# Kernel tuning notes

Measured on AMD Instinct MI355X. Metric: run time of the kernel, lower is better.

## Reference

```python
import jax, jax.numpy as jnp
import numpy as np

PAD, BOS, EOS = 0, 1, 2
VOCAB, EMB, HID, BATCH, MAXLEN = 32, 64, 1024, 2048, 100


def setup_inputs() -> dict:
    key = jax.random.key(0)
    ks = jax.random.split(key, 11)
    s = 0.08  # small init scale keeps softmax/sigmoid in a sane range
    g = lambda k, shape: (s * jax.random.normal(k, shape)).astype(jnp.float32)
    emb = g(ks[0], (VOCAB, EMB)).at[PAD].set(0.0)  # padding_idx row = 0
    return {
        "prevs": jnp.full((BATCH, 1), BOS, dtype=jnp.int32),
        "emb": emb,
        "Wih0": g(ks[1], (4 * HID, EMB)),
        "Whh0": g(ks[2], (4 * HID, HID)),
        "bih0": g(ks[3], (4 * HID,)),
        "bhh0": g(ks[4], (4 * HID,)),
        "Wih1": g(ks[5], (4 * HID, HID)),
        "Whh1": g(ks[6], (4 * HID, HID)),
        "bih1": g(ks[7], (4 * HID,)),
        "bhh1": g(ks[8], (4 * HID,)),
        "Wout": g(ks[9], (VOCAB, HID)),
        "bout": g(ks[10], (VOCAB,)),
        "max_len": MAXLEN,
    }


def _lstm_cell(x, h, c, Wih, Whh, bih, bhh):
    # torch LSTM gate order: i, f, g, o
    gates = x @ Wih.T + bih + h @ Whh.T + bhh  # [n, 4H]
    i, f, g, o = jnp.split(gates, 4, axis=-1)
    c = jax.nn.sigmoid(f) * c + jax.nn.sigmoid(i) * jnp.tanh(g)
    h = jax.nn.sigmoid(o) * jnp.tanh(c)
    return h, c


def reference(prevs, emb, Wih0, Whh0, bih0, bhh0, Wih1, Whh1, bih1, bhh1,
              Wout, bout, max_len):
    n = prevs.shape[0]
    H = Whh0.shape[1]
    prev = prevs[:, 0].astype(jnp.int32)
    h0 = jnp.zeros((n, H), jnp.float32)
    c0 = jnp.zeros((n, H), jnp.float32)
    h1 = jnp.zeros((n, H), jnp.float32)
    c1 = jnp.zeros((n, H), jnp.float32)
    is_end = prev == EOS
    lengths = jnp.zeros((n,), jnp.int32)
    keys = jax.random.split(jax.random.key(42), max_len)

    def step(carry, k):
        prev, h0, c0, h1, c1, is_end, lengths = carry
        x = emb[prev]                                   # [n, E]
        h0, c0 = _lstm_cell(x, h0, c0, Wih0, Whh0, bih0, bhh0)
        h1, c1 = _lstm_cell(h0, h1, c1, Wih1, Whh1, bih1, bhh1)
        logits = h1 @ Wout.T + bout                     # [n, V]
        cur = jax.random.categorical(k, logits).astype(jnp.int32)
        cur = jnp.where(is_end, PAD, cur)               # finished rows emit PAD
        lengths = lengths + (~is_end).astype(jnp.int32)
        is_end = is_end | (cur == EOS)
        return (cur, h0, c0, h1, c1, is_end, lengths), cur

    carry, seq = jax.lax.scan(step, (prev, h0, c0, h1, c1, is_end, lengths), keys)
    lengths = carry[6] + 1                               # +1 for BOS, as in sample_tensor
    sequences = jnp.concatenate([prevs.astype(jnp.int32), seq.T], axis=1)  # [n, 1+max_len]
    return sequences, lengths
```

## Files before the change

### kernel.cpp

```cpp
#include <hip/hip_runtime.h>
#include <cstdint>
#include <cstddef>


constexpr int PAD_TOK = 0, BOS_TOK = 1, EOS_TOK = 2;
constexpr int VOCAB = 32, EMB = 64, HID = 1024, BATCH = 2048, MAXLEN = 100;
constexpr int BK = 32;
constexpr int NKT_H = HID / BK;
constexpr float SCALE = 64.0f;
constexpr double INV_S2 = 1.0 / 4096.0;

using half8 = __attribute__((ext_vector_type(8))) _Float16;
using f32x4 = __attribute__((ext_vector_type(4))) float;
typedef unsigned short u16;
typedef uint32_t u32;

__device__ __forceinline__ u32 rotl32(u32 v, int d) {
  return (v << d) | (v >> (32 - d));
}

__device__ __forceinline__ void threefry2x32(u32 k0, u32 k1, u32 x0, u32 x1,
                                             u32& y0, u32& y1) {
  const u32 k2 = k0 ^ k1 ^ 0x1BD11BDAu;
#define TF_ROUND(r) do { x0 += x1; x1 = rotl32(x1, (r)); x1 ^= x0; } while (0)
  x0 += k0; x1 += k1;
  TF_ROUND(13); TF_ROUND(15); TF_ROUND(26); TF_ROUND(6);
  x0 += k1; x1 += k2 + 1u;
  TF_ROUND(17); TF_ROUND(29); TF_ROUND(16); TF_ROUND(24);
  x0 += k2; x1 += k0 + 2u;
  TF_ROUND(13); TF_ROUND(15); TF_ROUND(26); TF_ROUND(6);
  x0 += k0; x1 += k1 + 3u;
  TF_ROUND(17); TF_ROUND(29); TF_ROUND(16); TF_ROUND(24);
  x0 += k1; x1 += k2 + 4u;
  TF_ROUND(13); TF_ROUND(15); TF_ROUND(26); TF_ROUND(6);
  x0 += k2; x1 += k0 + 5u;
#undef TF_ROUND
  y0 = x0; y1 = x1;
}

__device__ __forceinline__ double rcp1p(double q) {
  const double d = 1.0 + q;
  double r = (double)__builtin_amdgcn_rcpf((float)d);
  r = r * fma(-d, r, 2.0);
  r = r * fma(-d, r, 2.0);
  return r;
}
__device__ __forceinline__ double exp2d(double t) {
  const double n = rint(t);
  const double f = t - n;
  double p = 1.0178086009239699e-07;
  p = fma(p, f, 1.3215542443841225e-06);
  p = fma(p, f, 1.5252733804059840e-05);
  p = fma(p, f, 1.5403530393381610e-04);
  p = fma(p, f, 1.3333558146428443e-03);
  p = fma(p, f, 9.6181291076284772e-03);
  p = fma(p, f, 5.5504108664821580e-02);
  p = fma(p, f, 2.4022650695910071e-01);
  p = fma(p, f, 6.9314718055994531e-01);
  p = fma(p, f, 1.0);
  const long long e = ((long long)(int)n + 1023) << 52;
  return p * __longlong_as_double(e);
}
__device__ __forceinline__ double sigd(double x) {
  return rcp1p(exp2d(x * -1.4426950408889634));
}
__device__ __forceinline__ double tanhd(double x) {
  return fma(2.0, rcp1p(exp2d(x * -2.8853900817779268)), -1.0);
}

__global__ __launch_bounds__(256) void pack_w(
    const float* __restrict__ src, int K, int nkt,
    uint4* __restrict__ dhi, uint4* __restrict__ dlo, int nchunks) {
  const int g = blockIdx.x * 256 + threadIdx.x;
  if (g >= nchunks) return;
  const int ut = g / (nkt * 512);
  const int rem = g - ut * (nkt * 512);
  const int kt = rem >> 9;
  const int slot = rem & 511;
  const int fm = slot >> 6, kg = (slot >> 4) & 3, r15 = slot & 15;
  const int row = (fm & 3) * HID + ut * 32 + (fm >> 2) * 16 + r15;
  const int col = kt * 32 + kg * 8;
  const float* s = src + (size_t)row * K + col;
  u16 hh[8], ll[8];
#pragma unroll
  for (int e = 0; e < 8; ++e) {
    const float x = s[e] * SCALE;
    const _Float16 h = (_Float16)x;
    const float rm = x - (float)h;
    const _Float16 l = (_Float16)rm;
    hh[e] = __builtin_bit_cast(u16, h);
    ll[e] = __builtin_bit_cast(u16, l);
  }
  dhi[g] = make_uint4((u32)hh[0] | ((u32)hh[1] << 16),
                      (u32)hh[2] | ((u32)hh[3] << 16),
                      (u32)hh[4] | ((u32)hh[5] << 16),
                      (u32)hh[6] | ((u32)hh[7] << 16));
  dlo[g] = make_uint4((u32)ll[0] | ((u32)ll[1] << 16),
                      (u32)ll[2] | ((u32)ll[3] << 16),
                      (u32)ll[4] | ((u32)ll[5] << 16),
                      (u32)ll[6] | ((u32)ll[7] << 16));
}

__global__ __launch_bounds__(256) void split_kernel(
    const float* __restrict__ src, u16* __restrict__ hi, u16* __restrict__ lo,
    int n) {
  const int i = blockIdx.x * 256 + threadIdx.x;
  if (i >= n) return;
  const float x = src[i] * SCALE;
  const _Float16 h = (_Float16)x;
  const float rem = x - (float)h;
  const _Float16 l = (_Float16)rem;
  hi[i] = __builtin_bit_cast(u16, h);
  lo[i] = __builtin_bit_cast(u16, l);
}

__global__ __launch_bounds__(256) void init_kernel(
    const int* __restrict__ prevs, float* __restrict__ c0,
    float* __restrict__ c1, u16* __restrict__ h0hi0, u16* __restrict__ h0lo0,
    u16* __restrict__ h0hi1, u16* __restrict__ h0lo1,
    u16* __restrict__ h1hi0, u16* __restrict__ h1lo0,
    u16* __restrict__ h1hi1, u16* __restrict__ h1lo1,
    int* __restrict__ prev, int* __restrict__ is_end,
    int* __restrict__ lengths, u32* __restrict__ keys,
    int* __restrict__ out_tok) {
  const int tid = blockIdx.x * 256 + threadIdx.x;
  const int total = BATCH * HID;
  if (tid < total) {
    c0[tid] = 0.0f; c1[tid] = 0.0f;
    h0hi0[tid] = 0; h0lo0[tid] = 0; h0hi1[tid] = 0; h0lo1[tid] = 0;
    h1hi0[tid] = 0; h1lo0[tid] = 0; h1hi1[tid] = 0; h1lo1[tid] = 0;
  }
  if (tid < BATCH) {
    const int p = prevs[tid];
    prev[tid] = p;
    is_end[tid] = (p == EOS_TOK) ? 1 : 0;
    lengths[tid] = 0;
    out_tok[(size_t)tid * (MAXLEN + 1)] = p;
  }
  if (tid < MAXLEN) {
    u32 y0, y1;
    threefry2x32(0u, 42u, 0u, (u32)tid, y0, y1);
    keys[2 * tid] = y0;
    keys[2 * tid + 1] = y1;
  }
}

template <bool GATHER, bool WRITE_F32>
__global__ __launch_bounds__(512, 2) void lstm_mfma(
    const uint4* __restrict__ A0p_hi, const uint4* __restrict__ A0p_lo,
    const u16* __restrict__ Ehi, const u16* __restrict__ Elo,
    const int* __restrict__ ptok, int nk0,
    const uint4* __restrict__ A1p_hi, const uint4* __restrict__ A1p_lo,
    const uint4* __restrict__ W0hi, const uint4* __restrict__ W0lo,
    const uint4* __restrict__ W1hi, const uint4* __restrict__ W1lo,
    const float* __restrict__ bih, const float* __restrict__ bhh,
    float* __restrict__ Cst, float* __restrict__ Hf32,
    uint4* __restrict__ Hp_hi, uint4* __restrict__ Hp_lo) {
  __shared__ uint4 lds4[2560];
  char* lds = (char*)lds4;

  const int tid = threadIdx.x;
  const int lane = tid & 63;
  const int wid = tid >> 6;
  const int wm = wid >> 1, wn = wid & 1;

  const int bid = blockIdx.x;
  const int mt = bid & 7;
  const int ut = bid >> 3;
  const int u0 = ut * 32;
  const int row0 = mt * 256;

  const int r15 = lane & 15;
  const int kgrp = lane >> 4;

  int tok4[4];
  if (GATHER) {
#pragma unroll
    for (int mi = 0; mi < 4; ++mi)
      tok4[mi] = ptok[row0 + (wm * 4 + mi) * 16 + r15];
  }

  const int NT = nk0 + NKT_H;

  auto loadT = [&](int kt, uint4* Ah, uint4* Al, uint4* Bh, uint4* Bl) {
    const bool s0 = kt < nk0;
    const int ktl = s0 ? kt : kt - nk0;
    const uint4* wh = s0 ? W0hi : W1hi;
    const uint4* wl = s0 ? W0lo : W1lo;
    const int wb = (ut * (s0 ? nk0 : NKT_H) + ktl) * 512 + wn * 256 + lane;
#pragma unroll
    for (int ni = 0; ni < 4; ++ni) {
      Bh[ni] = wh[wb + ni * 64];
      Bl[ni] = wl[wb + ni * 64];
    }
    if (GATHER && s0) {
#pragma unroll
      for (int mi = 0; mi < 4; ++mi) {
        const size_t ao = (size_t)tok4[mi] * EMB + ktl * 32 + kgrp * 8;
        Ah[mi] = *(const uint4*)(Ehi + ao);
        Al[mi] = *(const uint4*)(Elo + ao);
      }
    } else {
      const uint4* ah_ = s0 ? A0p_hi : A1p_hi;
      const uint4* al_ = s0 ? A0p_lo : A1p_lo;
      const int ab = (mt * NKT_H + ktl) * 1024 + wm * 256 + lane;
#pragma unroll
      for (int mi = 0; mi < 4; ++mi) {
        Ah[mi] = ah_[ab + mi * 64];
        Al[mi] = al_[ab + mi * 64];
      }
    }
  };

  f32x4 acc[4][4] = {};

  auto computeT = [&](const uint4* AhF, const uint4* AlF, const uint4* BhF,
                      const uint4* BlF) {
    half8 ah[4], al[4], bh[4], bl[4];
#pragma unroll
    for (int i = 0; i < 4; ++i) {
      ah[i] = __builtin_bit_cast(half8, AhF[i]);
      al[i] = __builtin_bit_cast(half8, AlF[i]);
      bh[i] = __builtin_bit_cast(half8, BhF[i]);
      bl[i] = __builtin_bit_cast(half8, BlF[i]);
    }
#pragma unroll
    for (int ni = 0; ni < 4; ++ni)
#pragma unroll
      for (int mi = 0; mi < 4; ++mi)
        acc[mi][ni] = __builtin_amdgcn_mfma_f32_16x16x32_f16(
            ah[mi], bh[ni], acc[mi][ni], 0, 0, 0);
#pragma unroll
    for (int ni = 0; ni < 4; ++ni)
#pragma unroll
      for (int mi = 0; mi < 4; ++mi)
        acc[mi][ni] = __builtin_amdgcn_mfma_f32_16x16x32_f16(
            ah[mi], bl[ni], acc[mi][ni], 0, 0, 0);
#pragma unroll
    for (int ni = 0; ni < 4; ++ni)
#pragma unroll
      for (int mi = 0; mi < 4; ++mi)
        acc[mi][ni] = __builtin_amdgcn_mfma_f32_16x16x32_f16(
            al[mi], bh[ni], acc[mi][ni], 0, 0, 0);
  };

  uint4 Ah0[4], Al0[4], Bh0[4], Bl0[4];
  uint4 Ah1[4], Al1[4], Bh1[4], Bl1[4];
  loadT(0, Ah0, Al0, Bh0, Bl0);
  loadT(1, Ah1, Al1, Bh1, Bl1);
#pragma unroll 1
  for (int t = 0; t < NT; t += 2) {
    computeT(Ah0, Al0, Bh0, Bl0);
    if (t + 2 < NT) loadT(t + 2, Ah0, Al0, Bh0, Bl0);
    computeT(Ah1, Al1, Bh1, Bl1);
    if (t + 3 < NT) loadT(t + 3, Ah1, Al1, Bh1, Bl1);
  }

  const int u_loc = wn * 16 + r15;
  const int u = u0 + u_loc;
  double bsum[4];
#pragma unroll
  for (int g = 0; g < 4; ++g)
    bsum[g] = (double)bih[g * HID + u] + (double)bhh[g * HID + u];

  float* Cb = Cst + (size_t)(mt * 32 + ut) * 8192;
  u16* hhT = (u16*)lds;
  u16* hlT = (u16*)(lds + 20480);
  const int hi4 = lane >> 4;

#pragma unroll
  for (int mi = 0; mi < 4; ++mi) {
#pragma unroll
    for (int r = 0; r < 4; ++r) {
      const int row = wm * 64 + mi * 16 + hi4 * 4 + r;
      const double gI = (double)acc[mi][0][r] * INV_S2 + bsum[0];
      const double gF = (double)acc[mi][1][r] * INV_S2 + bsum[1];
      const double gG = (double)acc[mi][2][r] * INV_S2 + bsum[2];
      const double gO = (double)acc[mi][3][r] * INV_S2 + bsum[3];
      const double ii = sigd(gI);
      const double ff = sigd(gF);
      const double gt = tanhd(gG);
      const double oo = sigd(gO);
      const int co = row * 32 + u_loc;
      const double cn = ff * (double)Cb[co] + ii * gt;
      Cb[co] = (float)cn;
      const float hf = (float)(oo * tanhd(cn));
      if (WRITE_F32) Hf32[(size_t)(row0 + row) * HID + u] = hf;
      const float hs = hf * SCALE;
      const _Float16 hh = (_Float16)hs;
      const float rm = hs - (float)hh;
      const _Float16 hl = (_Float16)rm;
      hhT[row * 40 + u_loc] = __builtin_bit_cast(u16, hh);
      hlT[row * 40 + u_loc] = __builtin_bit_cast(u16, hl);
    }
  }
  __syncthreads();

  const size_t mtut = ((size_t)mt * NKT_H + ut) * 1024;
#pragma unroll
  for (int j = 0; j < 2; ++j) {
    const int g = tid + j * 512;
    const int fA = g >> 6, kg = (g >> 4) & 3, rr = g & 15;
    const int row = fA * 16 + rr;
    const uint4 vh = *(const uint4*)(hhT + row * 40 + kg * 8);
    const uint4 vl = *(const uint4*)(hlT + row * 40 + kg * 8);
    Hp_hi[mtut + g] = vh;
    Hp_lo[mtut + g] = vl;
  }
}

__global__ __launch_bounds__(256) void sample_kernel(
    const float* __restrict__ h1, const float* __restrict__ Wout,
    const float* __restrict__ bout, const u32* __restrict__ keys, int t,
    int* __restrict__ prev, int* __restrict__ is_end, int* __restrict__ lengths,
    int* __restrict__ out_tok, int* __restrict__ len_out) {
  const int wave = threadIdx.x >> 6;
  const int lane = threadIdx.x & 63;
  const int row = (blockIdx.x & 7) * 256 + (blockIdx.x >> 3) * 4 + wave;
  const int v = lane & 31;
  const int half = lane >> 5;

  const float* hseg = h1 + (size_t)row * HID + half * (HID / 2);
  const float* wseg = Wout + (size_t)v * HID + half * (HID / 2);

  double acc = 0.0;
#pragma unroll 4
  for (int k = 0; k < HID / 2; k += 4) {
    const float4 w = *(const float4*)(wseg + k);
    const float4 h = *(const float4*)(hseg + k);
    acc = fma((double)w.x, (double)h.x, acc);
    acc = fma((double)w.y, (double)h.y, acc);
    acc = fma((double)w.z, (double)h.z, acc);
    acc = fma((double)w.w, (double)h.w, acc);
  }
  acc += __shfl_xor(acc, 32);

  const u32 k0 = keys[2 * t], k1 = keys[2 * t + 1];
  u32 y0, y1;
  threefry2x32(k0, k1, 0u, (u32)(row * VOCAB + v), y0, y1);
  const u32 bits = y0 ^ y1;
  const float f = __uint_as_float((bits >> 9) | 0x3f800000u) - 1.0f;
  const float uu = fmaxf(f, 1.17549435e-38f);
  const double g = -log(-log((double)uu));

  double z = acc + (double)bout[v] + g;
  int idx = v;
#pragma unroll
  for (int m = 1; m < 32; m <<= 1) {
    const double zo = __shfl_xor(z, m);
    const int io = __shfl_xor(idx, m);
    if (zo > z || (zo == z && io < idx)) { z = zo; idx = io; }
  }

  if (lane == 0) {
    const int e = is_end[row];
    const int cur = e ? PAD_TOK : idx;
    const int len = lengths[row] + (e ? 0 : 1);
    const int enew = e | (cur == EOS_TOK ? 1 : 0);
    prev[row] = cur;
    is_end[row] = enew;
    lengths[row] = len;
    out_tok[(size_t)row * (MAXLEN + 1) + t + 1] = cur;
    if (len_out) len_out[row] = len + 1;
  }
}

extern "C" void kernel_launch(void* const* d_in, const int* in_sizes, int n_in,
                              void* d_out, int out_size, void* d_ws,
                              size_t ws_size, hipStream_t stream) {
  const int* prevs = (const int*)d_in[0];
  const float* emb = (const float*)d_in[1];
  const float* Wih0 = (const float*)d_in[2];
  const float* Whh0 = (const float*)d_in[3];
  const float* bih0 = (const float*)d_in[4];
  const float* bhh0 = (const float*)d_in[5];
  const float* Wih1 = (const float*)d_in[6];
  const float* Whh1 = (const float*)d_in[7];
  const float* bih1 = (const float*)d_in[8];
  const float* bhh1 = (const float*)d_in[9];
  const float* Wout = (const float*)d_in[10];
  const float* bout = (const float*)d_in[11];

  const size_t SH = (size_t)BATCH * HID;
  const size_t CH = SH / 8;
  const size_t CW = (size_t)32 * NKT_H * 512;
  const size_t CW0 = (size_t)32 * 2 * 512;

  float* c0 = (float*)d_ws;
  float* c1 = c0 + SH;
  float* h1f = c1 + SH;
  uint4* q = (uint4*)(h1f + SH);
  uint4* ph0hi[2] = {q, q + CH};
  uint4* ph0lo[2] = {q + 2 * CH, q + 3 * CH};
  uint4* ph1hi[2] = {q + 4 * CH, q + 5 * CH};
  uint4* ph1lo[2] = {q + 6 * CH, q + 7 * CH};
  uint4* pw = q + 8 * CH;
  uint4* pwih0h = pw;              uint4* pwih0l = pwih0h + CW0;
  uint4* pwhh0h = pwih0l + CW0;    uint4* pwhh0l = pwhh0h + CW;
  uint4* pwih1h = pwhh0l + CW;     uint4* pwih1l = pwih1h + CW;
  uint4* pwhh1h = pwih1l + CW;     uint4* pwhh1l = pwhh1h + CW;
  u16* embh = (u16*)(pwhh1l + CW);
  u16* embl = embh + VOCAB * EMB;
  int* prev = (int*)(embl + VOCAB * EMB);
  int* is_end = prev + BATCH;
  int* lengths = is_end + BATCH;
  u32* keys = (u32*)(lengths + BATCH);

  int* out_tok = (int*)d_out;
  int* len_out = out_tok + (size_t)BATCH * (MAXLEN + 1);

  init_kernel<<<dim3((BATCH * HID) / 256), 256, 0, stream>>>(
      prevs, c0, c1, (u16*)ph0hi[0], (u16*)ph0lo[0], (u16*)ph0hi[1],
      (u16*)ph0lo[1], (u16*)ph1hi[0], (u16*)ph1lo[0], (u16*)ph1hi[1],
      (u16*)ph1lo[1], prev, is_end, lengths, keys, out_tok);

  split_kernel<<<dim3((VOCAB * EMB + 255) / 256), 256, 0, stream>>>(
      emb, embh, embl, VOCAB * EMB);
  pack_w<<<dim3((int)((CW0 + 255) / 256)), 256, 0, stream>>>(
      Wih0, EMB, 2, pwih0h, pwih0l, (int)CW0);
  pack_w<<<dim3((int)((CW + 255) / 256)), 256, 0, stream>>>(
      Whh0, HID, NKT_H, pwhh0h, pwhh0l, (int)CW);
  pack_w<<<dim3((int)((CW + 255) / 256)), 256, 0, stream>>>(
      Wih1, HID, NKT_H, pwih1h, pwih1l, (int)CW);
  pack_w<<<dim3((int)((CW + 255) / 256)), 256, 0, stream>>>(
      Whh1, HID, NKT_H, pwhh1h, pwhh1l, (int)CW);

  int p = 0;
  for (int t = 0; t < MAXLEN; ++t) {
    lstm_mfma<true, false><<<dim3(256), 512, 0, stream>>>(
        nullptr, nullptr, embh, embl, prev, 2, ph0hi[p], ph0lo[p],
        pwih0h, pwih0l, pwhh0h, pwhh0l, bih0, bhh0, c0, nullptr,
        ph0hi[p ^ 1], ph0lo[p ^ 1]);
    lstm_mfma<false, true><<<dim3(256), 512, 0, stream>>>(
        ph0hi[p ^ 1], ph0lo[p ^ 1], nullptr, nullptr, nullptr, NKT_H,
        ph1hi[p], ph1lo[p], pwih1h, pwih1l, pwhh1h, pwhh1l, bih1, bhh1,
        c1, h1f, ph1hi[p ^ 1], ph1lo[p ^ 1]);
    sample_kernel<<<dim3(BATCH / 4), 256, 0, stream>>>(
        h1f, Wout, bout, keys, t, prev, is_end, lengths, out_tok,
        (t == MAXLEN - 1) ? len_out : nullptr);
    p ^= 1;
  }
  (void)in_sizes; (void)n_in; (void)out_size; (void)ws_size;
}
```

Before: 21.00 ms.

## Stage LSTM weight tiles into LDS via async global_load_lds six-deep ring

New measurement: 18.87 ms. 10.1% less time.

```diff
diff --git a/kernel.cpp b/kernel.cpp
--- a/kernel.cpp
+++ b/kernel.cpp
@@ -38,6 +38,12 @@
   y0 = x0; y1 = x1;
 }
 
+__device__ __forceinline__ void gl_lds16(const void* g, void* l) {
+  __builtin_amdgcn_global_load_lds(
+      (const __attribute__((address_space(1))) void*)g,
+      (__attribute__((address_space(3))) void*)l, 16, 0, 0);
+}
+
 __device__ __forceinline__ double rcp1p(double q) {
   const double d = 1.0 + q;
   double r = (double)__builtin_amdgcn_rcpf((float)d);
@@ -146,7 +152,7 @@
 }
 
 template <bool GATHER, bool WRITE_F32>
-__global__ __launch_bounds__(512, 2) void lstm_mfma(
+__global__ __launch_bounds__(512) void lstm_mfma(
     const uint4* __restrict__ A0p_hi, const uint4* __restrict__ A0p_lo,
     const u16* __restrict__ Ehi, const u16* __restrict__ Elo,
     const int* __restrict__ ptok, int nk0,
@@ -156,7 +162,7 @@
     const float* __restrict__ bih, const float* __restrict__ bhh,
     float* __restrict__ Cst, float* __restrict__ Hf32,
     uint4* __restrict__ Hp_hi, uint4* __restrict__ Hp_lo) {
-  __shared__ uint4 lds4[2560];
+  __shared__ uint4 lds4[6144];
   char* lds = (char*)lds4;
 
   const int tid = threadIdx.x;
@@ -181,18 +187,26 @@
   }
 
   const int NT = nk0 + NKT_H;
-
-  auto loadT = [&](int kt, uint4* Ah, uint4* Al, uint4* Bh, uint4* Bl) {
+  const int G = NT / 2;
+
+  auto ldsW = [&](int buf, int pl, int slot) -> char* {
+    return lds + buf * 16384 + pl * 8192 + slot * 16;
+  };
+
+  auto stageW = [&](int kt) {
     const bool s0 = kt < nk0;
     const int ktl = s0 ? kt : kt - nk0;
     const uint4* wh = s0 ? W0hi : W1hi;
     const uint4* wl = s0 ? W0lo : W1lo;
-    const int wb = (ut * (s0 ? nk0 : NKT_H) + ktl) * 512 + wn * 256 + lane;
-#pragma unroll
-    for (int ni = 0; ni < 4; ++ni) {
-      Bh[ni] = wh[wb + ni * 64];
-      Bl[ni] = wl[wb + ni * 64];
-    }
+    const int wbase = (ut * (s0 ? nk0 : NKT_H) + ktl) * 512 + wid * 64;
+    const int buf = kt % 6;
+    gl_lds16(wh + wbase + lane, ldsW(buf, 0, wid * 64));
+    gl_lds16(wl + wbase + lane, ldsW(buf, 1, wid * 64));
+  };
+
+  auto loadA = [&](int kt, uint4* Ah, uint4* Al) {
+    const bool s0 = kt < nk0;
+    const int ktl = s0 ? kt : kt - nk0;
     if (GATHER && s0) {
 #pragma unroll
       for (int mi = 0; mi < 4; ++mi) {
@@ -214,15 +228,18 @@
 
   f32x4 acc[4][4] = {};
 
-  auto computeT = [&](const uint4* AhF, const uint4* AlF, const uint4* BhF,
-                      const uint4* BlF) {
+  auto computeT = [&](int kt, const uint4* AhF, const uint4* AlF) {
+    const int buf = kt % 6;
     half8 ah[4], al[4], bh[4], bl[4];
 #pragma unroll
     for (int i = 0; i < 4; ++i) {
       ah[i] = __builtin_bit_cast(half8, AhF[i]);
       al[i] = __builtin_bit_cast(half8, AlF[i]);
-      bh[i] = __builtin_bit_cast(half8, BhF[i]);
-      bl[i] = __builtin_bit_cast(half8, BlF[i]);
+    }
+#pragma unroll
+    for (int ni = 0; ni < 4; ++ni) {
+      bh[ni] = *(const half8*)ldsW(buf, 0, (wn * 4 + ni) * 64 + lane);
+      bl[ni] = *(const half8*)ldsW(buf, 1, (wn * 4 + ni) * 64 + lane);
     }
 #pragma unroll
     for (int ni = 0; ni < 4; ++ni)
@@ -244,17 +261,47 @@
             al[mi], bh[ni], acc[mi][ni], 0, 0, 0);
   };
 
-  uint4 Ah0[4], Al0[4], Bh0[4], Bl0[4];
-  uint4 Ah1[4], Al1[4], Bh1[4], Bl1[4];
-  loadT(0, Ah0, Al0, Bh0, Bl0);
-  loadT(1, Ah1, Al1, Bh1, Bl1);
+  uint4 Ah0[4], Al0[4], Ah1[4], Al1[4];
+
+  loadA(0, Ah0, Al0);
+  loadA(1, Ah1, Al1);
+#pragma unroll
+  for (int t = 0; t < 6; ++t) stageW(t);
+  asm volatile("s_waitcnt vmcnt(0)" ::: "memory");
+  __builtin_amdgcn_sched_barrier(0);
+  __builtin_amdgcn_s_barrier();
+
 #pragma unroll 1
-  for (int t = 0; t < NT; t += 2) {
-    computeT(Ah0, Al0, Bh0, Bl0);
-    if (t + 2 < NT) loadT(t + 2, Ah0, Al0, Bh0, Bl0);
-    computeT(Ah1, Al1, Bh1, Bl1);
-    if (t + 3 < NT) loadT(t + 3, Ah1, Al1, Bh1, Bl1);
-  }
+  for (int g = 0; g + 3 < G; ++g) {
+    const int t = 2 * g;
+    computeT(t, Ah0, Al0);
+    loadA(t + 2, Ah0, Al0);
+    computeT(t + 1, Ah1, Al1);
+    loadA(t + 3, Ah1, Al1);
+    asm volatile("s_waitcnt vmcnt(36)" ::: "memory");
+    __builtin_amdgcn_sched_barrier(0);
+    __builtin_amdgcn_s_barrier();
+    stageW(t + 6);
+    stageW(t + 7);
+  }
+
+  asm volatile("s_waitcnt vmcnt(0)" ::: "memory");
+  __builtin_amdgcn_sched_barrier(0);
+  __builtin_amdgcn_s_barrier();
+  {
+    const int t = 2 * G - 6;
+    computeT(t, Ah0, Al0);
+    loadA(t + 2, Ah0, Al0);
+    computeT(t + 1, Ah1, Al1);
+    loadA(t + 3, Ah1, Al1);
+    computeT(t + 2, Ah0, Al0);
+    loadA(t + 4, Ah0, Al0);
+    computeT(t + 3, Ah1, Al1);
+    loadA(t + 5, Ah1, Al1);
+    computeT(t + 4, Ah0, Al0);
+    computeT(t + 5, Ah1, Al1);
+  }
+  __syncthreads();
 
   const int u_loc = wn * 16 + r15;
   const int u = u0 + u_loc;
```
